# Performance work log

Measured on AMD Instinct MI355X. Metric: run time of the kernel, lower is better.

The kernel has to match this reference:

```python
import jax, jax.numpy as jnp
import numpy as np

WD, WH, WW = 2, 7, 7
N = WD * WH * WW          # 98 tokens per window
DIM = 128
HEADS = 4
HEAD_DIM = DIM // HEADS   # 32
B_ = 2048                 # num_windows * batch
NW = 64                   # windows per image (mask leading dim)
TABLE = (2 * WD - 1) * (2 * WH - 1) * (2 * WW - 1)  # 507


def _relative_position_index():
    coords = np.stack(np.meshgrid(np.arange(WD), np.arange(WH), np.arange(WW), indexing='ij'))
    flat = coords.reshape(3, -1)                     # [3, N]
    rel = flat[:, :, None] - flat[:, None, :]        # [3, N, N]
    rel = rel.transpose(1, 2, 0).copy()              # [N, N, 3]
    rel[:, :, 0] += WD - 1
    rel[:, :, 1] += WH - 1
    rel[:, :, 2] += WW - 1
    rel[:, :, 0] *= (2 * WH - 1) * (2 * WW - 1)
    rel[:, :, 1] *= 2 * WW - 1
    return rel.sum(-1).astype(np.int32)             # [N, N]


def setup_inputs() -> dict:
    key = jax.random.key(0)
    ks = jax.random.split(key, 6)
    x = jax.random.normal(ks[0], (B_, N, DIM), dtype=jnp.float32)
    mask = jax.random.normal(ks[1], (NW, N, N), dtype=jnp.float32)
    qkv_w = jax.random.normal(ks[2], (3 * DIM, DIM), dtype=jnp.float32) * 0.02
    qkv_b = jnp.zeros((3 * DIM,), dtype=jnp.float32)
    proj_w = jax.random.normal(ks[3], (DIM, DIM), dtype=jnp.float32) * 0.02
    proj_b = jnp.zeros((DIM,), dtype=jnp.float32)
    bias_table = jax.random.normal(ks[4], (TABLE, HEADS), dtype=jnp.float32) * 0.02
    rel_idx = jnp.asarray(_relative_position_index())
    return {"x": x, "mask": mask, "qkv_w": qkv_w, "qkv_b": qkv_b,
            "proj_w": proj_w, "proj_b": proj_b, "bias_table": bias_table,
            "rel_idx": rel_idx}


def reference(x, mask, qkv_w, qkv_b, proj_w, proj_b, bias_table, rel_idx):
    b, n, c = x.shape
    hd = c // HEADS
    scale = hd ** -0.5
    qkv = x @ qkv_w.T + qkv_b                          # [B_, N, 3C]
    qkv = qkv.reshape(b, n, 3, HEADS, hd)
    qkv = jnp.transpose(qkv, (2, 0, 3, 1, 4))          # [3, B_, H, N, hd]
    q, k, v = qkv[0], qkv[1], qkv[2]
    attn = jnp.einsum('bhnd,bhmd->bhnm', q * scale, k)  # [B_, H, N, N]
    # gathered relative position bias
    bias = bias_table[rel_idx.reshape(-1)].reshape(n, n, HEADS)
    bias = jnp.transpose(bias, (2, 0, 1))               # [H, N, N]
    attn = attn + bias[None]
    nw = mask.shape[0]
    attn = attn.reshape(b // nw, nw, HEADS, n, n) + mask[None, :, None]
    attn = jax.nn.softmax(attn.reshape(b, HEADS, n, n), axis=-1)
    out = jnp.einsum('bhnm,bhmd->bnhd', attn, v).reshape(b, n, c)
    out = out @ proj_w.T + proj_b
    return out
```

## Files before the change

kernel.cpp:

```cpp
#include <hip/hip_runtime.h>
#include <stdint.h>

#define NTOK 98
#define DIM 128
#define HEADS 4
#define HD 32
#define BWIN 2048
#define NW 64
#define SCALE 0.17677669529663687f
#define QSTR 32
#define VSTR 104

typedef __bf16 bf16_t;
typedef bf16_t bf16x8 __attribute__((ext_vector_type(8)));
typedef float f32x4 __attribute__((ext_vector_type(4)));
typedef unsigned short u16;
typedef unsigned int u32;
typedef unsigned long long u64;

__device__ __forceinline__ u16 f2bf(float f) {
    union { bf16_t h; u16 u; } v; v.h = (bf16_t)f; return v.u;
}
__device__ __forceinline__ float bf2f(u16 b) {
    union { u16 u; bf16_t h; } v; v.u = b; return (float)v.h;
}
__device__ __forceinline__ int qk_idx(int row, int d) {
    return row * QSTR + ((((d >> 3) ^ (row & 3)) << 3) | (d & 7));
}

__global__ void k0_prep(const float* __restrict__ qkv_w, const float* __restrict__ proj_w,
                        const float* __restrict__ mask,
                        const float* __restrict__ bias_table, const int* __restrict__ rel_idx,
                        const float* __restrict__ x,
                        u16* __restrict__ qkvw_bf, u16* __restrict__ pw_bf,
                        u16* __restrict__ mbT, u16* __restrict__ xbf)
{
    int t = blockIdx.x * 256 + threadIdx.x;
    if (t < 49152) {
        qkvw_bf[t] = f2bf(qkv_w[t]);
    } else if (t < 65536) {
        int r = t - 49152;
        pw_bf[r] = f2bf(proj_w[r]);
    } else if (t < 3276800) {
        int r = t - 65536;
        int w    = r / 50176;
        int rem  = r - w * 50176;
        int hh   = rem / 12544;
        int rem2 = rem - hh * 12544;
        int i    = rem2 >> 7;
        int c    = rem2 & 127;
        int l16  = c >> 3;
        int njp  = c & 7;
        int j    = njp * 16 + l16;
        float val = -1e30f;
        if (njp < 7 && j < NTOK)
            val = mask[w * 9604 + i * NTOK + j] + bias_table[rel_idx[i * NTOK + j] * HEADS + hh];
        mbT[r] = f2bf(val);
    } else if (t < 6488064) {
        size_t idx = (size_t)(t - 3276800) * 8;
        const float4 a0 = *reinterpret_cast<const float4*>(x + idx);
        const float4 a1 = *reinterpret_cast<const float4*>(x + idx + 4);
        u64 p0 = (u64)f2bf(a0.x) | ((u64)f2bf(a0.y) << 16) |
                 ((u64)f2bf(a0.z) << 32) | ((u64)f2bf(a0.w) << 48);
        u64 p1 = (u64)f2bf(a1.x) | ((u64)f2bf(a1.y) << 16) |
                 ((u64)f2bf(a1.z) << 32) | ((u64)f2bf(a1.w) << 48);
        *reinterpret_cast<u64*>(&xbf[idx])     = p0;
        *reinterpret_cast<u64*>(&xbf[idx + 4]) = p1;
    }
}

__global__ __launch_bounds__(256, 5) void k_attn(
    const u16* __restrict__ xbf, const u16* __restrict__ qkvw_bf,
    const float* __restrict__ qkv_b, const u16* __restrict__ mbT,
    u16* __restrict__ OG)
{
    __shared__ __align__(16) u16 qL[NTOK * QSTR];
    __shared__ __align__(16) u16 kL[NTOK * QSTR];
    __shared__ __align__(16) u16 vL[HD * VSTR];
    __shared__ __align__(16) u16 Pscr[4][16 * VSTR];

    const int bh   = (blockIdx.x & 7) * 1024 + (blockIdx.x >> 3);
    const int b    = bh >> 2;
    const int h    = bh & 3;
    const int tid  = threadIdx.x;
    const int wave = tid >> 6;
    const int lane = tid & 63;
    const int l16  = lane & 15;
    const int quad = lane >> 4;

    const u16* xb = xbf + (size_t)b * (NTOK * DIM);

    {
        const int u0 = (wave * 21) >> 2;
        const int u1 = ((wave + 1) * 21) >> 2;
        int cached = -1;
        bf16x8 Bf[2][4];
        float  cb[2];
        for (int u = u0; u < u1; ++u) {
            const int part = u / 7;
            const int mt   = u - part * 7;
            if (part != cached) {
                const u16* wp = qkvw_bf + (size_t)part * DIM * DIM;
#pragma unroll
                for (int nt2 = 0; nt2 < 2; ++nt2) {
                    const int col = h * HD + nt2 * 16 + l16;
#pragma unroll
                    for (int ks = 0; ks < 4; ++ks)
                        Bf[nt2][ks] = *reinterpret_cast<const bf16x8*>(
                            wp + col * DIM + quad * 8 + ks * 32);
                    cb[nt2] = qkv_b[part * DIM + col];
                }
                cached = part;
            }
            int arow = mt * 16 + l16;
            if (arow > 97) arow = 97;
            bf16x8 af[4];
#pragma unroll
            for (int ks = 0; ks < 4; ++ks)
                af[ks] = *reinterpret_cast<const bf16x8*>(
                    xb + arow * DIM + quad * 8 + ks * 32);
            f32x4 acc0 = {0.f, 0.f, 0.f, 0.f};
            f32x4 acc1 = {0.f, 0.f, 0.f, 0.f};
            __builtin_amdgcn_s_setprio(1);
#pragma unroll
            for (int ks = 0; ks < 4; ++ks) {
                acc0 = __builtin_amdgcn_mfma_f32_16x16x32_bf16(af[ks], Bf[0][ks], acc0, 0, 0, 0);
                acc1 = __builtin_amdgcn_mfma_f32_16x16x32_bf16(af[ks], Bf[1][ks], acc1, 0, 0, 0);
            }
            __builtin_amdgcn_s_setprio(0);
            const int tokb = mt * 16 + quad * 4;
#pragma unroll
            for (int nt2 = 0; nt2 < 2; ++nt2) {
                const f32x4& acc = nt2 ? acc1 : acc0;
                const int d = nt2 * 16 + l16;
                const float cbv = cb[nt2];
                if (part == 0) {
#pragma unroll
                    for (int reg = 0; reg < 4; ++reg) {
                        int tok = tokb + reg;
                        if (tok < NTOK)
                            qL[qk_idx(tok, d)] = f2bf((acc[reg] + cbv) * SCALE);
                    }
                } else if (part == 1) {
#pragma unroll
                    for (int reg = 0; reg < 4; ++reg) {
                        int tok = tokb + reg;
                        if (tok < NTOK)
                            kL[qk_idx(tok, d)] = f2bf(acc[reg] + cbv);
                    }
                } else {
                    u16* vrow = &vL[d * VSTR];
                    if (tokb + 3 <= 97) {
                        u64 pack = 0;
#pragma unroll
                        for (int reg = 0; reg < 4; ++reg)
                            pack |= ((u64)f2bf(acc[reg] + cbv)) << (16 * reg);
                        *reinterpret_cast<u64*>(&vrow[tokb]) = pack;
                    } else if (tokb <= 97) {
                        u32 pack = (u32)f2bf(acc[0] + cbv) | ((u32)f2bf(acc[1] + cbv) << 16);
                        *reinterpret_cast<u32*>(&vrow[tokb]) = pack;
                    }
                }
            }
        }
    }
    __syncthreads();

    {
        const u16* mbtp = mbT + ((size_t)((b & (NW - 1)) * HEADS + h)) * (NTOK * 128);
        u16* ps = &Pscr[wave][0];
        const int qko = ((quad ^ (l16 & 3)) << 3);

        bf16x8 kf[7];
#pragma unroll
        for (int nj = 0; nj < 7; ++nj) {
            int krow = nj * 16 + l16;
            if (krow > 97) krow = 97;
            kf[nj] = *reinterpret_cast<const bf16x8*>(&kL[krow * QSTR + qko]);
        }

        auto softmax_tile = [&](const f32x4* sacc, const bf16x8* mrows, float* rin) {
#pragma unroll
            for (int reg = 0; reg < 4; ++reg) {
                float s[7];
#pragma unroll
                for (int nj = 0; nj < 7; ++nj)
                    s[nj] = sacc[nj][reg] + (float)mrows[reg][nj];
                float mx = fmaxf(fmaxf(fmaxf(s[0], s[1]), fmaxf(s[2], s[3])),
                                 fmaxf(fmaxf(s[4], s[5]), s[6]));
#pragma unroll
                for (int off = 1; off < 16; off <<= 1) mx = fmaxf(mx, __shfl_xor(mx, off));
                float p[7];
                float lsum = 0.f;
#pragma unroll
                for (int nj = 0; nj < 7; ++nj) {
                    p[nj] = __expf(s[nj] - mx);
                    lsum += p[nj];
                }
                u16* psr = &ps[(quad * 4 + reg) * VSTR];
#pragma unroll
                for (int nj = 0; nj < 6; ++nj)
                    psr[nj * 16 + l16] = f2bf(p[nj]);
                if (l16 < 8) psr[96 + l16] = f2bf(p[6]);
#pragma unroll
                for (int off = 1; off < 16; off <<= 1) lsum += __shfl_xor(lsum, off);
                rin[reg] = 1.f / lsum;
            }
        };

        auto pv_store = [&](int mt, const float* rin) {
            bf16x8 pf[3];
#pragma unroll
            for (int ks = 0; ks < 3; ++ks)
                pf[ks] = *reinterpret_cast<const bf16x8*>(&ps[l16 * VSTR + quad * 8 + ks * 32]);
#pragma unroll
            for (int nt = 0; nt < 2; ++nt) {
                f32x4 oacc = {0.f, 0.f, 0.f, 0.f};
                __builtin_amdgcn_s_setprio(1);
#pragma unroll
                for (int ks = 0; ks < 3; ++ks) {
                    bf16x8 vf = *reinterpret_cast<const bf16x8*>(
                        &vL[(nt * 16 + l16) * VSTR + quad * 8 + ks * 32]);
                    oacc = __builtin_amdgcn_mfma_f32_16x16x32_bf16(pf[ks], vf, oacc, 0, 0, 0);
                }
                __builtin_amdgcn_s_setprio(0);
                int d = nt * 16 + l16;
                float v96 = bf2f(vL[d * VSTR + 96]);
                float v97 = bf2f(vL[d * VSTR + 97]);
#pragma unroll
                for (int reg = 0; reg < 4; ++reg) {
                    int i = mt * 16 + quad * 4 + reg;
                    if (i < NTOK) {
                        float p96 = bf2f(ps[(quad * 4 + reg) * VSTR + 96]);
                        float p97 = bf2f(ps[(quad * 4 + reg) * VSTR + 97]);
                        OG[((size_t)b * NTOK + i) * DIM + h * HD + d] =
                            f2bf((oacc[reg] + p96 * v96 + p97 * v97) * rin[reg]);
                    }
                }
            }
        };

        const int mt1 = wave;
        const int mt2 = wave + 4;
        const bool has2 = (mt2 < 7);

        bf16x8 mrows1[4];
#pragma unroll
        for (int reg = 0; reg < 4; ++reg) {
            int i = mt1 * 16 + quad * 4 + reg;
            mrows1[reg] = *reinterpret_cast<const bf16x8*>(&mbtp[i * 128 + l16 * 8]);
        }
        bf16x8 qf1 = *reinterpret_cast<const bf16x8*>(&qL[(mt1 * 16 + l16) * QSTR + qko]);
        f32x4 sacc1[7];
        __builtin_amdgcn_s_setprio(1);
#pragma unroll
        for (int nj = 0; nj < 7; ++nj) {
            f32x4 z = {0.f, 0.f, 0.f, 0.f};
            sacc1[nj] = __builtin_amdgcn_mfma_f32_16x16x32_bf16(qf1, kf[nj], z, 0, 0, 0);
        }
        __builtin_amdgcn_s_setprio(0);

        float rin1[4];
        softmax_tile(sacc1, mrows1, rin1);

        f32x4 sacc2[7];
        bf16x8 mrows2[4];
        if (has2) {
            int qrow2 = mt2 * 16 + l16;
            if (qrow2 > 97) qrow2 = 97;
            bf16x8 qf2 = *reinterpret_cast<const bf16x8*>(&qL[qrow2 * QSTR + qko]);
            __builtin_amdgcn_s_setprio(1);
#pragma unroll
            for (int nj = 0; nj < 7; ++nj) {
                f32x4 z = {0.f, 0.f, 0.f, 0.f};
                sacc2[nj] = __builtin_amdgcn_mfma_f32_16x16x32_bf16(qf2, kf[nj], z, 0, 0, 0);
            }
            __builtin_amdgcn_s_setprio(0);
#pragma unroll
            for (int reg = 0; reg < 4; ++reg) {
                int i  = mt2 * 16 + quad * 4 + reg;
                int ic = (i > 97) ? 97 : i;
                mrows2[reg] = *reinterpret_cast<const bf16x8*>(&mbtp[ic * 128 + l16 * 8]);
            }
        }

        pv_store(mt1, rin1);
        if (has2) {
            float rin2[4];
            softmax_tile(sacc2, mrows2, rin2);
            pv_store(mt2, rin2);
        }
    }
}

__global__ __launch_bounds__(256, 6) void k_proj(
    const u16* __restrict__ OG, const u16* __restrict__ pw_bf,
    const float* __restrict__ proj_b, float* __restrict__ out)
{
    __shared__ __align__(16) u16 A[98 * 136];

    const int b    = ((blockIdx.x & 7) << 8) + (blockIdx.x >> 3);
    const int tid  = threadIdx.x;
    const int wave = tid >> 6;
    const int lane = tid & 63;
    const int l16  = lane & 15;
    const int quad = lane >> 4;

    bf16x8 bw[2][4];
    float  pb[2];
#pragma unroll
    for (int nt2 = 0; nt2 < 2; ++nt2) {
        const int col = (wave * 2 + nt2) * 16 + l16;
#pragma unroll
        for (int ks = 0; ks < 4; ++ks)
            bw[nt2][ks] = *reinterpret_cast<const bf16x8*>(
                pw_bf + col * DIM + quad * 8 + ks * 32);
        pb[nt2] = proj_b[col];
    }

    const u16* ob = OG + (size_t)b * (NTOK * DIM);
    for (int idx = tid; idx < (NTOK * DIM / 8); idx += 256) {
        int row = idx >> 4;
        int c8  = idx & 15;
        *reinterpret_cast<bf16x8*>(&A[row * 136 + c8 * 8]) =
            *reinterpret_cast<const bf16x8*>(ob + row * DIM + c8 * 8);
    }
    __syncthreads();

    for (int mt = 0; mt < 7; ++mt) {
        int arow = mt * 16 + l16;
        if (arow > 97) arow = 97;
        bf16x8 af[4];
#pragma unroll
        for (int ks = 0; ks < 4; ++ks)
            af[ks] = *reinterpret_cast<const bf16x8*>(&A[arow * 136 + quad * 8 + ks * 32]);
        f32x4 acc0 = {0.f, 0.f, 0.f, 0.f};
        f32x4 acc1 = {0.f, 0.f, 0.f, 0.f};
#pragma unroll
        for (int ks = 0; ks < 4; ++ks) {
            acc0 = __builtin_amdgcn_mfma_f32_16x16x32_bf16(af[ks], bw[0][ks], acc0, 0, 0, 0);
            acc1 = __builtin_amdgcn_mfma_f32_16x16x32_bf16(af[ks], bw[1][ks], acc1, 0, 0, 0);
        }
#pragma unroll
        for (int nt2 = 0; nt2 < 2; ++nt2) {
            const f32x4& acc = nt2 ? acc1 : acc0;
            const int col = (wave * 2 + nt2) * 16 + l16;
#pragma unroll
            for (int reg = 0; reg < 4; ++reg) {
                int row = mt * 16 + quad * 4 + reg;
                if (row < NTOK)
                    out[((size_t)b * NTOK + row) * DIM + col] = acc[reg] + pb[nt2];
            }
        }
    }
}

extern "C" void kernel_launch(void* const* d_in, const int* in_sizes, int n_in,
                              void* d_out, int out_size, void* d_ws, size_t ws_size,
                              hipStream_t stream)
{
    const float* x       = (const float*)d_in[0];
    const float* mask    = (const float*)d_in[1];
    const float* qkv_w   = (const float*)d_in[2];
    const float* qkv_b   = (const float*)d_in[3];
    const float* proj_w  = (const float*)d_in[4];
    const float* proj_b  = (const float*)d_in[5];
    const float* bias_tb = (const float*)d_in[6];
    const int*   rel_idx = (const int*)d_in[7];
    float* out = (float*)d_out;

    char* ws = (char*)d_ws;
    u16* qkvw_bf = (u16*)(ws + 0);
    u16* pw_bf   = (u16*)(ws + 98304);
    u16* mbT     = (u16*)(ws + 131072);
    u16* xbf     = (u16*)(ws + 6553600);
    u16* OG      = (u16*)(ws + 57933824);

    k0_prep<<<25344, 256, 0, stream>>>(qkv_w, proj_w, mask, bias_tb, rel_idx, x,
                                       qkvw_bf, pw_bf, mbT, xbf);
    k_attn<<<BWIN * HEADS, 256, 0, stream>>>(xbf, qkvw_bf, qkv_b, mbT, OG);
    k_proj<<<BWIN, 256, 0, stream>>>(OG, pw_bf, proj_b, out);
}
```

Before: 356.1 us.

## Fold log2e into Q and mask, drop softmax max pass, store head-major output

```diff
diff --git a/kernel.cpp b/kernel.cpp
--- a/kernel.cpp
+++ b/kernel.cpp
@@ -8,6 +8,7 @@
 #define BWIN 2048
 #define NW 64
 #define SCALE 0.17677669529663687f
+#define LOG2E 1.4426950408889634f
 #define QSTR 32
 #define VSTR 104
 
@@ -54,7 +55,8 @@
         int j    = njp * 16 + l16;
         float val = -1e30f;
         if (njp < 7 && j < NTOK)
-            val = mask[w * 9604 + i * NTOK + j] + bias_table[rel_idx[i * NTOK + j] * HEADS + hh];
+            val = LOG2E * (mask[w * 9604 + i * NTOK + j]
+                           + bias_table[rel_idx[i * NTOK + j] * HEADS + hh]);
         mbT[r] = f2bf(val);
     } else if (t < 6488064) {
         size_t idx = (size_t)(t - 3276800) * 8;
@@ -139,7 +141,7 @@
                     for (int reg = 0; reg < 4; ++reg) {
                         int tok = tokb + reg;
                         if (tok < NTOK)
-                            qL[qk_idx(tok, d)] = f2bf((acc[reg] + cbv) * SCALE);
+                            qL[qk_idx(tok, d)] = f2bf((acc[reg] + cbv) * (SCALE * LOG2E));
                     }
                 } else if (part == 1) {
 #pragma unroll
@@ -182,29 +184,19 @@
         auto softmax_tile = [&](const f32x4* sacc, const bf16x8* mrows, float* rin) {
 #pragma unroll
             for (int reg = 0; reg < 4; ++reg) {
-                float s[7];
+                float p[7];
 #pragma unroll
                 for (int nj = 0; nj < 7; ++nj)
-                    s[nj] = sacc[nj][reg] + (float)mrows[reg][nj];
-                float mx = fmaxf(fmaxf(fmaxf(s[0], s[1]), fmaxf(s[2], s[3])),
-                                 fmaxf(fmaxf(s[4], s[5]), s[6]));
-#pragma unroll
-                for (int off = 1; off < 16; off <<= 1) mx = fmaxf(mx, __shfl_xor(mx, off));
-                float p[7];
-                float lsum = 0.f;
-#pragma unroll
-                for (int nj = 0; nj < 7; ++nj) {
-                    p[nj] = __expf(s[nj] - mx);
-                    lsum += p[nj];
-                }
+                    p[nj] = __builtin_amdgcn_exp2f(sacc[nj][reg] + (float)mrows[reg][nj]);
                 u16* psr = &ps[(quad * 4 + reg) * VSTR];
 #pragma unroll
                 for (int nj = 0; nj < 6; ++nj)
                     psr[nj * 16 + l16] = f2bf(p[nj]);
                 if (l16 < 8) psr[96 + l16] = f2bf(p[6]);
+                float lsum = ((p[0] + p[1]) + (p[2] + p[3])) + ((p[4] + p[5]) + p[6]);
 #pragma unroll
                 for (int off = 1; off < 16; off <<= 1) lsum += __shfl_xor(lsum, off);
-                rin[reg] = 1.f / lsum;
+                rin[reg] = __builtin_amdgcn_rcpf(lsum);
             }
         };
 
@@ -233,7 +225,7 @@
                     if (i < NTOK) {
                         float p96 = bf2f(ps[(quad * 4 + reg) * VSTR + 96]);
                         float p97 = bf2f(ps[(quad * 4 + reg) * VSTR + 97]);
-                        OG[((size_t)b * NTOK + i) * DIM + h * HD + d] =
+                        OG[((size_t)bh * NTOK + i) * HD + d] =
                             f2bf((oacc[reg] + p96 * v96 + p97 * v97) * rin[reg]);
                     }
                 }
@@ -266,6 +258,7 @@
         f32x4 sacc2[7];
         bf16x8 mrows2[4];
         if (has2) {
+            __builtin_amdgcn_sched_barrier(0);
             int qrow2 = mt2 * 16 + l16;
             if (qrow2 > 97) qrow2 = 97;
             bf16x8 qf2 = *reinterpret_cast<const bf16x8*>(&qL[qrow2 * QSTR + qko]);
@@ -282,6 +275,7 @@
                 int ic = (i > 97) ? 97 : i;
                 mrows2[reg] = *reinterpret_cast<const bf16x8*>(&mbtp[ic * 128 + l16 * 8]);
             }
+            __builtin_amdgcn_sched_barrier(0);
         }
 
         pv_store(mt1, rin1);
@@ -318,12 +312,14 @@
         pb[nt2] = proj_b[col];
     }
 
-    const u16* ob = OG + (size_t)b * (NTOK * DIM);
+    const u16* ob = OG + (size_t)b * (HEADS * NTOK * HD);
     for (int idx = tid; idx < (NTOK * DIM / 8); idx += 256) {
         int row = idx >> 4;
         int c8  = idx & 15;
+        int hh  = c8 >> 2;
+        int d8  = c8 & 3;
         *reinterpret_cast<bf16x8*>(&A[row * 136 + c8 * 8]) =
-            *reinterpret_cast<const bf16x8*>(ob + row * DIM + c8 * 8);
+            *reinterpret_cast<const bf16x8*>(ob + ((size_t)hh * NTOK + row) * HD + d8 * 8);
     }
     __syncthreads();
 
```

After: 352.3 us. About the same (-1.1%).
